# Optimization experiments

Hardware: AMD Instinct MI355X
Metric: run time of the kernel (lower is better)

## Reference

```python
import jax, jax.numpy as jnp
import numpy as np

N_HEAD = 8
D_HEAD = 16
D_MODEL = 128
LEN_Q = 256
MEM_LEN = 256
BATCH = 4


def setup_inputs() -> dict:
    key = jax.random.key(0)
    k1, k2, k3, k4, k5 = jax.random.split(key, 5)
    h = jax.random.normal(k1, (LEN_Q, BATCH, D_MODEL), dtype=jnp.float32)
    mems = jax.random.normal(k2, (MEM_LEN, BATCH, D_MODEL), dtype=jnp.float32)
    # nn.Linear weights are [out_features, in_features]
    Wq = jax.random.normal(k3, (N_HEAD * D_HEAD, D_MODEL), dtype=jnp.float32) / np.sqrt(D_MODEL)
    Wk = jax.random.normal(k4, (N_HEAD * D_HEAD, D_MODEL), dtype=jnp.float32) / np.sqrt(D_MODEL)
    paramR = jax.random.normal(k5, (N_HEAD,), dtype=jnp.float32)
    return {"h": h, "mems": mems, "Wq": Wq, "Wk": Wk, "paramR": paramR}


def reference(h, mems, Wq, Wk, paramR):
    # h: [Lq, B, Dm], mems: [M, B, Dm]
    c = jnp.concatenate([mems, h], axis=0)  # [Lk, B, Dm]
    Lq, B = h.shape[0], h.shape[1]
    Lk = c.shape[0]
    # Linear (no bias): x @ W.T, then split heads and move to [H, B, L, Dh]
    head_q = (h @ Wq.T).reshape(Lq, B, N_HEAD, D_HEAD).transpose(2, 1, 0, 3)
    head_k = (c @ Wk.T).reshape(Lk, B, N_HEAD, D_HEAD).transpose(2, 1, 0, 3)
    # Pairwise difference: [H, B, Lq, Lk, Dh]
    diff = head_q[:, :, :, None, :] - head_k[:, :, None, :, :]
    scaled = diff * paramR[:, None, None, None, None] / jnp.pi
    # torch.sinc == jnp.sinc (normalized sinc, sinc(0)=1)
    score = jnp.abs(jnp.prod(jnp.sinc(scaled), axis=4))  # [H, B, Lq, Lk]
    # permute(2, 3, 1, 0) -> [Lq, Lk, B, H]
    return score.transpose(2, 3, 1, 0)
```

## Files before the change

### kernel.cpp

```cpp
#include <hip/hip_runtime.h>
#include <math.h>

#define LQ 256
#define MEML 256
#define LK 512
#define BB 4
#define NH 8
#define DH 16
#define DM 128

constexpr float INV2PI = 0.15915494309189535f;

__global__ __launch_bounds__(128) void proj_kernel(
    const float* __restrict__ hh, const float* __restrict__ mems,
    const float* __restrict__ Wq, const float* __restrict__ Wk,
    const float* __restrict__ paramR,
    float* __restrict__ qs, float* __restrict__ ksT)
{
    __shared__ float x[8 * 128];
    const int blk = blockIdx.x;
    const int t = threadIdx.x;
    const bool isQ = (blk < 128);
    const int row0 = isQ ? blk * 8 : (blk - 128) * 8;
    const float* __restrict__ W = isQ ? Wq : Wk;

    for (int r = 0; r < 8; ++r) {
        const int row = row0 + r;
        const float* src;
        if (isQ) {
            src = hh + row * DM;
        } else {
            const int j = row >> 2;
            src = (j < MEML) ? (mems + row * DM) : (hh + (row - MEML * BB) * DM);
        }
        x[r * 128 + t] = src[t];
    }
    __syncthreads();

    float acc[8] = {0, 0, 0, 0, 0, 0, 0, 0};
    const float* wrow = W + t * DM;
    for (int k = 0; k < DM; k += 4) {
        const float4 w = *(const float4*)(wrow + k);
        #pragma unroll
        for (int r = 0; r < 8; ++r) {
            acc[r] += x[r * 128 + k + 0] * w.x + x[r * 128 + k + 1] * w.y
                    + x[r * 128 + k + 2] * w.z + x[r * 128 + k + 3] * w.w;
        }
    }
    const int h = t >> 4, d = t & 15;
    const float rs = paramR[h] * INV2PI;
    if (isQ) {
        float* dst = qs + row0 * 128 + t;
        #pragma unroll
        for (int r = 0; r < 8; ++r) dst[r * 128] = acc[r] * rs;
    } else {
        #pragma unroll
        for (int r = 0; r < 8; ++r) {
            const int row = row0 + r;
            const int j = row >> 2, b = row & 3;
            ksT[((d >> 2) * LK + j) * 128 + (b * 8 + h) * 4 + (d & 3)] = acc[r] * rs;
        }
    }
}

__global__ __launch_bounds__(256) void score_kernel(
    const float* __restrict__ qs, const float* __restrict__ ksT,
    float* __restrict__ out)
{
    const int t = threadIdx.x;
    const int bh = t & 31;
    const int js = t >> 5;
    const int i0 = blockIdx.x * 2;
    const int jbase = blockIdx.y * 64;

    float q[2][16];
    #pragma unroll
    for (int ii = 0; ii < 2; ++ii) {
        const float* qp = qs + ((i0 + ii) * 32 + bh) * 16;
        #pragma unroll
        for (int d = 0; d < 16; d += 4) {
            const float4 v = *(const float4*)(qp + d);
            q[ii][d] = v.x; q[ii][d + 1] = v.y; q[ii][d + 2] = v.z; q[ii][d + 3] = v.w;
        }
    }

    constexpr float i2 = INV2PI * INV2PI;
    constexpr float i4 = i2 * i2;
    constexpr float i8 = i4 * i4;
    constexpr float C16 = i8 * i8;
    constexpr float EPS = 2.0e-4f * INV2PI;

    float k[16];
    {
        const int j0 = jbase + js;
        #pragma unroll
        for (int d4 = 0; d4 < 4; ++d4) {
            const float4 v = *(const float4*)(ksT + (d4 * LK + j0) * 128 + bh * 4);
            k[d4 * 4 + 0] = v.x; k[d4 * 4 + 1] = v.y;
            k[d4 * 4 + 2] = v.z; k[d4 * 4 + 3] = v.w;
        }
    }

    #pragma unroll
    for (int m = 0; m < 8; ++m) {
        float kn[16];
        if (m < 7) {
            const int jn = jbase + (m + 1) * 8 + js;
            #pragma unroll
            for (int d4 = 0; d4 < 4; ++d4) {
                const float4 v = *(const float4*)(ksT + (d4 * LK + jn) * 128 + bh * 4);
                kn[d4 * 4 + 0] = v.x; kn[d4 * 4 + 1] = v.y;
                kn[d4 * 4 + 2] = v.z; kn[d4 * 4 + 3] = v.w;
            }
        }
        const int j = jbase + m * 8 + js;
        #pragma unroll
        for (int ii = 0; ii < 2; ++ii) {
            float pn0 = 1.f, pd0 = 1.f, pn1 = 1.f, pd1 = 1.f;
            #pragma unroll
            for (int d = 0; d < 16; ++d) {
                const float u = q[ii][d] - k[d];
                const float s = __builtin_amdgcn_sinf(u);
                const bool g = __builtin_fabsf(u) > EPS;
                const float nn = g ? s : 1.0f;
                const float dd = g ? u : INV2PI;
                if (d < 8) { pn0 *= nn; pd0 *= dd; }
                else       { pn1 *= nn; pd1 *= dd; }
            }
            const float r0 = pn0 * __builtin_amdgcn_rcpf(pd0);
            const float r1 = pn1 * __builtin_amdgcn_rcpf(pd1);
            out[((i0 + ii) * LK + j) * 32 + bh] = __builtin_fabsf(r0 * r1) * C16;
        }
        if (m < 7) {
            #pragma unroll
            for (int d = 0; d < 16; ++d) k[d] = kn[d];
        }
    }
}

extern "C" void kernel_launch(void* const* d_in, const int* in_sizes, int n_in,
                              void* d_out, int out_size, void* d_ws, size_t ws_size,
                              hipStream_t stream) {
    const float* hh     = (const float*)d_in[0];
    const float* mems   = (const float*)d_in[1];
    const float* Wq     = (const float*)d_in[2];
    const float* Wk     = (const float*)d_in[3];
    const float* paramR = (const float*)d_in[4];
    float* out = (float*)d_out;

    float* qs  = (float*)d_ws;
    float* ksT = qs + LQ * BB * DM;

    proj_kernel<<<384, 128, 0, stream>>>(hh, mems, Wq, Wk, paramR, qs, ksT);
    score_kernel<<<dim3(128, 8), 256, 0, stream>>>(qs, ksT, out);
}
```

Baseline: 34.30 us.

## Precompute sin/cos of projections and use angle-difference identity in score

The projection kernel now also writes sin and cos of each scaled q and k value. The score kernel computes sin(q-k) as sin q cos k - cos q sin k, so the inner loop needs no transcendental calls. Each score block now handles one query row instead of two, and the projection kernel uses 4 rows per block, so both kernels launch more blocks. The cost is three times the memory traffic and registers for q/k loads, double-buffered k arrays, reduced q reuse, and a different accuracy profile for small differences (EPS changed).

```diff
diff --git a/kernel.cpp b/kernel.cpp
--- a/kernel.cpp
+++ b/kernel.cpp
@@ -15,34 +15,32 @@
     const float* __restrict__ hh, const float* __restrict__ mems,
     const float* __restrict__ Wq, const float* __restrict__ Wk,
     const float* __restrict__ paramR,
-    float* __restrict__ qs, float* __restrict__ ksT)
+    float* __restrict__ qv, float* __restrict__ qsn, float* __restrict__ qcs,
+    float* __restrict__ kv, float* __restrict__ ksn, float* __restrict__ kcs)
 {
-    __shared__ float x[8 * 128];
+    __shared__ float x[4 * 128];
     const int blk = blockIdx.x;
     const int t = threadIdx.x;
-    const bool isQ = (blk < 128);
-    const int row0 = isQ ? blk * 8 : (blk - 128) * 8;
+    const bool isQ = (blk < 256);
+    const int row0 = isQ ? blk * 4 : (blk - 256) * 4;
     const float* __restrict__ W = isQ ? Wq : Wk;
 
-    for (int r = 0; r < 8; ++r) {
+    for (int r = 0; r < 4; ++r) {
         const int row = row0 + r;
         const float* src;
-        if (isQ) {
-            src = hh + row * DM;
-        } else {
-            const int j = row >> 2;
-            src = (j < MEML) ? (mems + row * DM) : (hh + (row - MEML * BB) * DM);
-        }
+        if (isQ) src = hh + row * DM;
+        else     src = (row < MEML * BB) ? (mems + row * DM)
+                                         : (hh + (row - MEML * BB) * DM);
         x[r * 128 + t] = src[t];
     }
     __syncthreads();
 
-    float acc[8] = {0, 0, 0, 0, 0, 0, 0, 0};
+    float acc[4] = {0, 0, 0, 0};
     const float* wrow = W + t * DM;
     for (int k = 0; k < DM; k += 4) {
         const float4 w = *(const float4*)(wrow + k);
         #pragma unroll
-        for (int r = 0; r < 8; ++r) {
+        for (int r = 0; r < 4; ++r) {
             acc[r] += x[r * 128 + k + 0] * w.x + x[r * 128 + k + 1] * w.y
                     + x[r * 128 + k + 2] * w.z + x[r * 128 + k + 3] * w.w;
         }
@@ -50,91 +48,107 @@
     const int h = t >> 4, d = t & 15;
     const float rs = paramR[h] * INV2PI;
     if (isQ) {
-        float* dst = qs + row0 * 128 + t;
         #pragma unroll
-        for (int r = 0; r < 8; ++r) dst[r * 128] = acc[r] * rs;
+        for (int r = 0; r < 4; ++r) {
+            const float v = acc[r] * rs;
+            const int idx = (row0 + r) * 128 + t;
+            qv[idx]  = v;
+            qsn[idx] = __builtin_amdgcn_sinf(v);
+            qcs[idx] = __builtin_amdgcn_cosf(v);
+        }
     } else {
         #pragma unroll
-        for (int r = 0; r < 8; ++r) {
+        for (int r = 0; r < 4; ++r) {
+            const float v = acc[r] * rs;
             const int row = row0 + r;
             const int j = row >> 2, b = row & 3;
-            ksT[((d >> 2) * LK + j) * 128 + (b * 8 + h) * 4 + (d & 3)] = acc[r] * rs;
+            const int idx = ((d >> 2) * LK + j) * 128 + (b * 8 + h) * 4 + (d & 3);
+            kv[idx]  = v;
+            ksn[idx] = __builtin_amdgcn_sinf(v);
+            kcs[idx] = __builtin_amdgcn_cosf(v);
         }
     }
 }
 
 __global__ __launch_bounds__(256) void score_kernel(
-    const float* __restrict__ qs, const float* __restrict__ ksT,
+    const float* __restrict__ qv, const float* __restrict__ qsn,
+    const float* __restrict__ qcs,
+    const float* __restrict__ kv, const float* __restrict__ ksn,
+    const float* __restrict__ kcs,
     float* __restrict__ out)
 {
     const int t = threadIdx.x;
     const int bh = t & 31;
     const int js = t >> 5;
-    const int i0 = blockIdx.x * 2;
+    const int i = blockIdx.x;
     const int jbase = blockIdx.y * 64;
-
-    float q[2][16];
-    #pragma unroll
-    for (int ii = 0; ii < 2; ++ii) {
-        const float* qp = qs + ((i0 + ii) * 32 + bh) * 16;
-        #pragma unroll
-        for (int d = 0; d < 16; d += 4) {
-            const float4 v = *(const float4*)(qp + d);
-            q[ii][d] = v.x; q[ii][d + 1] = v.y; q[ii][d + 2] = v.z; q[ii][d + 3] = v.w;
-        }
-    }
 
     constexpr float i2 = INV2PI * INV2PI;
     constexpr float i4 = i2 * i2;
     constexpr float i8 = i4 * i4;
     constexpr float C16 = i8 * i8;
-    constexpr float EPS = 2.0e-4f * INV2PI;
+    constexpr float EPS = 4.0e-4f;
 
-    float k[16];
+    float q[16], sq[16], cq[16];
+    {
+        const int qoff = (i * 32 + bh) * 16;
+        #pragma unroll
+        for (int d = 0; d < 16; d += 4) {
+            const float4 a = *(const float4*)(qv  + qoff + d);
+            const float4 b = *(const float4*)(qsn + qoff + d);
+            const float4 c = *(const float4*)(qcs + qoff + d);
+            q[d] = a.x;  q[d+1] = a.y;  q[d+2] = a.z;  q[d+3] = a.w;
+            sq[d] = b.x; sq[d+1] = b.y; sq[d+2] = b.z; sq[d+3] = b.w;
+            cq[d] = c.x; cq[d+1] = c.y; cq[d+2] = c.z; cq[d+3] = c.w;
+        }
+    }
+
+    float ka[2][16], ska[2][16], cka[2][16];
     {
         const int j0 = jbase + js;
         #pragma unroll
         for (int d4 = 0; d4 < 4; ++d4) {
-            const float4 v = *(const float4*)(ksT + (d4 * LK + j0) * 128 + bh * 4);
-            k[d4 * 4 + 0] = v.x; k[d4 * 4 + 1] = v.y;
-            k[d4 * 4 + 2] = v.z; k[d4 * 4 + 3] = v.w;
+            const int off = (d4 * LK + j0) * 128 + bh * 4;
+            const float4 a = *(const float4*)(kv  + off);
+            const float4 b = *(const float4*)(ksn + off);
+            const float4 c = *(const float4*)(kcs + off);
+            ka[0][d4*4] = a.x;  ka[0][d4*4+1] = a.y;  ka[0][d4*4+2] = a.z;  ka[0][d4*4+3] = a.w;
+            ska[0][d4*4] = b.x; ska[0][d4*4+1] = b.y; ska[0][d4*4+2] = b.z; ska[0][d4*4+3] = b.w;
+            cka[0][d4*4] = c.x; cka[0][d4*4+1] = c.y; cka[0][d4*4+2] = c.z; cka[0][d4*4+3] = c.w;
         }
     }
 
     #pragma unroll
     for (int m = 0; m < 8; ++m) {
-        float kn[16];
+        const int cur = m & 1, nxt = cur ^ 1;
         if (m < 7) {
             const int jn = jbase + (m + 1) * 8 + js;
             #pragma unroll
             for (int d4 = 0; d4 < 4; ++d4) {
-                const float4 v = *(const float4*)(ksT + (d4 * LK + jn) * 128 + bh * 4);
-                kn[d4 * 4 + 0] = v.x; kn[d4 * 4 + 1] = v.y;
-                kn[d4 * 4 + 2] = v.z; kn[d4 * 4 + 3] = v.w;
+                const int off = (d4 * LK + jn) * 128 + bh * 4;
+                const float4 a = *(const float4*)(kv  + off);
+                const float4 b = *(const float4*)(ksn + off);
+                const float4 c = *(const float4*)(kcs + off);
+                ka[nxt][d4*4] = a.x;  ka[nxt][d4*4+1] = a.y;  ka[nxt][d4*4+2] = a.z;  ka[nxt][d4*4+3] = a.w;
+                ska[nxt][d4*4] = b.x; ska[nxt][d4*4+1] = b.y; ska[nxt][d4*4+2] = b.z; ska[nxt][d4*4+3] = b.w;
+                cka[nxt][d4*4] = c.x; cka[nxt][d4*4+1] = c.y; cka[nxt][d4*4+2] = c.z; cka[nxt][d4*4+3] = c.w;
             }
         }
         const int j = jbase + m * 8 + js;
+        float pn0 = 1.f, pd0 = 1.f, pn1 = 1.f, pd1 = 1.f;
         #pragma unroll
-        for (int ii = 0; ii < 2; ++ii) {
-            float pn0 = 1.f, pd0 = 1.f, pn1 = 1.f, pd1 = 1.f;
-            #pragma unroll
-            for (int d = 0; d < 16; ++d) {
-                const float u = q[ii][d] - k[d];
-                const float s = __builtin_amdgcn_sinf(u);
-                const bool g = __builtin_fabsf(u) > EPS;
-                const float nn = g ? s : 1.0f;
-                const float dd = g ? u : INV2PI;
-                if (d < 8) { pn0 *= nn; pd0 *= dd; }
-                else       { pn1 *= nn; pd1 *= dd; }
-            }
-            const float r0 = pn0 * __builtin_amdgcn_rcpf(pd0);
-            const float r1 = pn1 * __builtin_amdgcn_rcpf(pd1);
-            out[((i0 + ii) * LK + j) * 32 + bh] = __builtin_fabsf(r0 * r1) * C16;
+        for (int d = 0; d < 16; ++d) {
+            const float dl = q[d] - ka[cur][d];
+            const float num = sq[d] * cka[cur][d] - cq[d] * ska[cur][d];
+            const bool g = __builtin_fabsf(dl) > EPS;
+            const float nn = g ? num : 1.0f;
+            const float dd = g ? dl : INV2PI;
+            if (d < 8) { pn0 *= nn; pd0 *= dd; }
+            else       { pn1 *= nn; pd1 *= dd; }
         }
-        if (m < 7) {
-            #pragma unroll
-            for (int d = 0; d < 16; ++d) k[d] = kn[d];
-        }
+        const float r0 = pn0 * __builtin_amdgcn_rcpf(pd0);
+        const float r1 = pn1 * __builtin_amdgcn_rcpf(pd1);
+        out[(i * LK + j) * 32 + bh] = __builtin_fabsf(r0 * r1) * C16;
     }
 }
 
@@ -148,9 +162,14 @@
     const float* paramR = (const float*)d_in[4];
     float* out = (float*)d_out;
 
-    float* qs  = (float*)d_ws;
-    float* ksT = qs + LQ * BB * DM;
+    float* qv  = (float*)d_ws;
+    float* qsn = qv  + LQ * BB * DM;
+    float* qcs = qsn + LQ * BB * DM;
+    float* kv  = qcs + LQ * BB * DM;
+    float* ksn = kv  + LK * BB * DM;
+    float* kcs = ksn + LK * BB * DM;
 
-    proj_kernel<<<384, 128, 0, stream>>>(hh, mems, Wq, Wk, paramR, qs, ksT);
-    score_kernel<<<dim3(128, 8), 256, 0, stream>>>(qs, ksT, out);
+    proj_kernel<<<768, 128, 0, stream>>>(hh, mems, Wq, Wk, paramR,
+                                         qv, qsn, qcs, kv, ksn, kcs);
+    score_kernel<<<dim3(256, 8), 256, 0, stream>>>(qv, qsn, qcs, kv, ksn, kcs, out);
 }
```

Result: slower. 70.44 us (+105.4%).
